# Kernel optimization log

Measured on AMD Instinct MI355X. Metric: run time of the kernel, lower is better.

The kernel has to match this reference:

```python
import jax, jax.numpy as jnp
import numpy as np

B, S, DIM, N, D = 1, 3072, 2048, 16, 128
EPS = 1e-06


def rms_norm(x, w, eps=EPS):
    # x: [B, S, C]; normalize over last dim (matches npu_rms_norm)
    var = jnp.mean(jnp.square(x), axis=-1, keepdims=True)
    return x * jax.lax.rsqrt(var + eps) * w


def rope_interleave(x, cos, sin):
    # x: [B, S, N, D]; cos/sin: [B, S, 1, D] with pairwise-repeated values.
    # interleave mode: (x0, x1) -> (x0*c - x1*s, x1*c + x0*s) for adjacent pairs.
    xe = x[..., 0::2]
    xo = x[..., 1::2]
    rot = jnp.stack([-xo, xe], axis=-1).reshape(x.shape)
    return (x * cos + rot * sin).astype(jnp.float32)  # rope_apply casts to float


def setup_inputs() -> dict:
    key = jax.random.key(0)
    ks = jax.random.split(key, 16)
    sd = 1.0 / np.sqrt(DIM)
    inp = {
        'x': jax.random.normal(ks[0], (B, S, DIM), jnp.float32),
        'Wq': jax.random.normal(ks[1], (DIM, DIM), jnp.float32) * sd,
        'bq': jax.random.normal(ks[2], (DIM,), jnp.float32) * 0.01,
        'Wk': jax.random.normal(ks[3], (DIM, DIM), jnp.float32) * sd,
        'bk': jax.random.normal(ks[4], (DIM,), jnp.float32) * 0.01,
        'Wv': jax.random.normal(ks[5], (DIM, DIM), jnp.float32) * sd,
        'bv': jax.random.normal(ks[6], (DIM,), jnp.float32) * 0.01,
        'Wo': jax.random.normal(ks[7], (DIM, DIM), jnp.float32) * sd,
        'bo': jax.random.normal(ks[8], (DIM,), jnp.float32) * 0.01,
        'norm_q_w': jnp.ones((DIM,), jnp.float32),
        'norm_k_w': jnp.ones((DIM,), jnp.float32),
    }
    # per-sample 3D rope folded into precomputed interleaved cos/sin tables
    pos = jnp.arange(S, dtype=jnp.float32)
    inv = 1.0 / (10000.0 ** (jnp.arange(D // 2, dtype=jnp.float32) / (D // 2)))
    ang = pos[:, None] * inv[None, :]                    # [S, D/2]
    cos = jnp.repeat(jnp.cos(ang), 2, axis=-1)           # [S, D] pairwise repeated
    sin = jnp.repeat(jnp.sin(ang), 2, axis=-1)
    inp['rope_cos'] = jnp.broadcast_to(cos[None, :, None, :], (B, S, 1, D))
    inp['rope_sin'] = jnp.broadcast_to(sin[None, :, None, :], (B, S, 1, D))
    inp['seq_lens'] = jax.random.randint(ks[9], (B,), S // 2, S + 1).astype(jnp.int32)
    inp['grid_sizes'] = jnp.broadcast_to(jnp.array([[12, 16, 16]], jnp.int32), (B, 3))
    return inp


def reference(x, Wq, bq, Wk, bk, Wv, bv, Wo, bo, norm_q_w, norm_k_w,
              rope_cos, rope_sin, seq_lens, grid_sizes):
    b, s, _ = x.shape
    # fused QKV projection + RMSNorm on q/k
    q = rms_norm(x @ Wq.T + bq, norm_q_w).reshape(b, s, N, D)
    k = rms_norm(x @ Wk.T + bk, norm_k_w).reshape(b, s, N, D)
    v = (x @ Wv.T + bv).reshape(b, s, N, D)
    # per-sample interleaved RoPE (outputs float32, as in rope_apply)
    q = rope_interleave(q, rope_cos, rope_sin)
    k = rope_interleave(k, rope_cos, rope_sin)
    # full attention with key-length masking (window_size = (-1, -1))
    scale = 1.0 / np.sqrt(D)
    scores = jnp.einsum('bqnd,bknd->bnqk', q, k) * scale    # [B, N, S, S]
    kmask = jnp.arange(s)[None, :] < seq_lens[:, None]       # [B, S]
    scores = jnp.where(kmask[:, None, None, :], scores, jnp.float32(-1e30))
    probs = jax.nn.softmax(scores, axis=-1)
    out = jnp.einsum('bnqk,bknd->bqnd', probs, v.astype(jnp.float32))
    out = out.reshape(b, s, N * D)
    return out @ Wo.T + bo
```

## Files before the change

kernel.cpp:

```cpp
#include <hip/hip_runtime.h>
#include <hip/hip_bf16.h>

typedef __attribute__((ext_vector_type(8))) short short8;
typedef __attribute__((ext_vector_type(4))) float f32x4;

#define SQ 3072
#define DM 2048
#define NHEAD 16
#define HDIM 128

__device__ __forceinline__ unsigned short f2bf(float f) {
  union { float f; unsigned int u; } un; un.f = f;
  unsigned int r = un.u + 0x7fffu + ((un.u >> 16) & 1u);
  return (unsigned short)(r >> 16);
}

__device__ __forceinline__ unsigned short f2bf_hw(float f) {
  __hip_bfloat16 h = __float2bfloat16(f);
  return *reinterpret_cast<unsigned short*>(&h);
}

__device__ __forceinline__ void gload_lds16(const void* g, void* l) {
  __builtin_amdgcn_global_load_lds(
      (const __attribute__((address_space(1))) void*)g,
      (__attribute__((address_space(3))) void*)l, 16, 0, 0);
}

__global__ __launch_bounds__(256) void cvt_all(
    const float* __restrict__ x, const float* __restrict__ wq, const float* __restrict__ wk,
    const float* __restrict__ wv, const float* __restrict__ wo,
    unsigned short* __restrict__ xb, unsigned short* __restrict__ wqkvb,
    unsigned short* __restrict__ wob)
{
  int b = blockIdx.x;
  const float* src; unsigned short* dst; int idx;
  if (b < 3072) { src = x; dst = xb; idx = b; }
  else {
    int r = b - 3072; int w = r >> 11; idx = r & 2047;
    src = (w == 0) ? wq : (w == 1) ? wk : (w == 2) ? wv : wo;
    dst = (w < 3) ? wqkvb + (size_t)w * DM * DM : wob;
  }
  int i = (idx * 256 + threadIdx.x) * 8;
  float4 a = *(const float4*)(src + i);
  float4 c = *(const float4*)(src + i + 4);
  short8 r;
  r[0] = (short)f2bf(a.x); r[1] = (short)f2bf(a.y);
  r[2] = (short)f2bf(a.z); r[3] = (short)f2bf(a.w);
  r[4] = (short)f2bf(c.x); r[5] = (short)f2bf(c.y);
  r[6] = (short)f2bf(c.z); r[7] = (short)f2bf(c.w);
  *(short8*)(dst + i) = r;
}

__global__ __launch_bounds__(512, 2) void gemm_nt_bias(
    const unsigned short* __restrict__ A, const unsigned short* __restrict__ B,
    const float* __restrict__ b0, const float* __restrict__ b1, const float* __restrict__ b2,
    float* __restrict__ C, int M, int N, int K, int nbm)
{
  __shared__ __align__(16) unsigned short lds[3 * 12288];
  const int tid = threadIdx.x;
  const int w = tid >> 6, l = tid & 63;
  const int wm = w >> 2, wn = w & 3;
  const int lr = l & 15, lg = l >> 4;

  const int nwg = gridDim.x;
  const int swz = (blockIdx.x & 7) * (nwg >> 3) + (blockIdx.x >> 3);
  const int m0 = (swz % nbm) * 128, n0 = (swz / nbm) * 256;

  const int srow = tid >> 2;
  const int scol = ((tid & 3) ^ ((tid >> 3) & 3)) * 8;
  const unsigned short* aS  = A + (size_t)(m0 + srow) * K + scol;
  const unsigned short* bS0 = B + (size_t)(n0 + srow) * K + scol;
  const unsigned short* bS1 = B + (size_t)(n0 + 128 + srow) * K + scol;
  const int ldst = w * 512;

  auto stage = [&](int t, int b) {
    unsigned short* base = &lds[b * 12288];
    const size_t tc = (size_t)t * 32;
    gload_lds16(aS + tc, base + ldst);
    gload_lds16(bS0 + tc, base + 4096 + ldst);
    gload_lds16(bS1 + tc, base + 8192 + ldst);
  };

  const int sx = ((lr >> 1) & 3);
  const int aoff = (wm * 64 + lr) * 32 + ((lg ^ sx) * 8);
  const int boff = 4096 + (wn * 64 + lr) * 32 + ((lg ^ sx) * 8);

  f32x4 acc[4][4] = {};
  const int nt = K >> 5;

  stage(0, 0); stage(1, 1);
  asm volatile("s_waitcnt vmcnt(3)" ::: "memory");
  __builtin_amdgcn_s_barrier();

  for (int t = 0; t < nt; ++t) {
    const unsigned short* buf = &lds[(t % 3) * 12288];
    if (t + 2 < nt) stage(t + 2, (t + 2) % 3);
    short8 af[4], bfr[4];
    #pragma unroll
    for (int m = 0; m < 4; ++m) af[m] = *(const short8*)&buf[aoff + m * 512];
    #pragma unroll
    for (int n = 0; n < 4; ++n) bfr[n] = *(const short8*)&buf[boff + n * 512];
    __builtin_amdgcn_s_setprio(1);
    #pragma unroll
    for (int m = 0; m < 4; ++m) {
      #pragma unroll
      for (int n = 0; n < 4; ++n)
        acc[m][n] = __builtin_amdgcn_mfma_f32_16x16x32_bf16(af[m], bfr[n], acc[m][n], 0, 0, 0);
    }
    __builtin_amdgcn_s_setprio(0);
    if (t + 2 < nt) {
      asm volatile("s_waitcnt vmcnt(3)" ::: "memory");
      __builtin_amdgcn_s_barrier();
    } else if (t + 2 == nt) {
      asm volatile("s_waitcnt vmcnt(0)" ::: "memory");
      __builtin_amdgcn_s_barrier();
    }
  }

  const float* bp = (n0 < DM) ? b0 : ((n0 < 2 * DM) ? b1 : b2);
  #pragma unroll
  for (int n = 0; n < 4; ++n) {
    int col = n0 + wn * 64 + n * 16 + lr;
    float bv = bp[col & (DM - 1)];
    #pragma unroll
    for (int m = 0; m < 4; ++m) {
      int row = m0 + wm * 64 + m * 16 + lg * 4;
      #pragma unroll
      for (int j = 0; j < 4; ++j)
        C[(size_t)(row + j) * N + col] = acc[m][n][j] + bv;
    }
  }
}

__global__ __launch_bounds__(256) void normrope(
    const float* __restrict__ qkv, const float* __restrict__ nqw, const float* __restrict__ nkw,
    const float* __restrict__ cosb, const float* __restrict__ sinb,
    unsigned short* __restrict__ Qb, unsigned short* __restrict__ Kb)
{
  const int s = blockIdx.x, z = blockIdx.y;
  const float* row = qkv + ((size_t)s * 3 + z) * DM;
  const float* gw = z ? nkw : nqw;
  unsigned short* ob = z ? Kb : Qb;
  const int t = threadIdx.x;
  float v[8];
  {
    float4 a = *(const float4*)(row + t * 8);
    float4 b = *(const float4*)(row + t * 8 + 4);
    v[0] = a.x; v[1] = a.y; v[2] = a.z; v[3] = a.w;
    v[4] = b.x; v[5] = b.y; v[6] = b.z; v[7] = b.w;
  }
  float ss = 0.f;
  #pragma unroll
  for (int i = 0; i < 8; ++i) ss += v[i] * v[i];
  #pragma unroll
  for (int off = 1; off < 64; off <<= 1) ss += __shfl_xor(ss, off);
  __shared__ float red[4];
  const int wave = t >> 6, lane = t & 63;
  if (lane == 0) red[wave] = ss;
  __syncthreads();
  float tot = red[0] + red[1] + red[2] + red[3];
  float rsc = rsqrtf(tot * (1.0f / 2048.0f) + 1e-6f);
  const float qs = z ? 1.0f : 0.12751879522087045f;
  const int col = t * 8, d = col & 127, h = col >> 7;
  const float* cb = cosb + (size_t)s * HDIM + d;
  const float* sb = sinb + (size_t)s * HDIM + d;
  float y[8];
  #pragma unroll
  for (int i = 0; i < 8; ++i) y[i] = v[i] * rsc * gw[col + i];
  short8 r;
  #pragma unroll
  for (int p = 0; p < 4; ++p) {
    float e = y[2 * p], o = y[2 * p + 1];
    float c0 = cb[2 * p], s0 = sb[2 * p];
    float c1 = cb[2 * p + 1], s1 = sb[2 * p + 1];
    r[2 * p]     = (short)f2bf((e * c0 - o * s0) * qs);
    r[2 * p + 1] = (short)f2bf((o * c1 + e * s1) * qs);
  }
  *(short8*)(ob + ((size_t)h * SQ + s) * HDIM + d) = r;
}

__global__ __launch_bounds__(256) void vtrans(const float* __restrict__ V, int ldv,
                                              unsigned short* __restrict__ Vt)
{
  __shared__ float tile[64][65];
  const int db = blockIdx.x * 64, sb = blockIdx.y * 64, h = blockIdx.z;
  const int t = threadIdx.x;
  const int rr = t >> 2, c0 = (t & 3) * 16;
  const float* src = V + (size_t)(sb + rr) * ldv + h * HDIM + db + c0;
  #pragma unroll
  for (int i = 0; i < 4; ++i) {
    float4 a = *(const float4*)(src + i * 4);
    tile[rr][c0 + i * 4 + 0] = a.x; tile[rr][c0 + i * 4 + 1] = a.y;
    tile[rr][c0 + i * 4 + 2] = a.z; tile[rr][c0 + i * 4 + 3] = a.w;
  }
  __syncthreads();
  const int dr = t >> 2, s0 = (t & 3) * 16;
  short8 r0, r1;
  #pragma unroll
  for (int i = 0; i < 8; ++i) r0[i] = (short)f2bf(tile[s0 + i][dr]);
  #pragma unroll
  for (int i = 0; i < 8; ++i) r1[i] = (short)f2bf(tile[s0 + 8 + i][dr]);
  unsigned short* dst = Vt + ((size_t)h * HDIM + db + dr) * SQ + sb + s0;
  *(short8*)(dst) = r0;
  *(short8*)(dst + 8) = r1;
}

#define PST 76
__global__ __launch_bounds__(256) void attn(
    const unsigned short* __restrict__ Qb, const unsigned short* __restrict__ Kb,
    const unsigned short* __restrict__ Vt, const int* __restrict__ seq_lens,
    unsigned short* __restrict__ aout)
{
  __shared__ __align__(16) unsigned short Ks[64 * 136];
  __shared__ __align__(16) unsigned short Vs[128 * 72];
  __shared__ __align__(16) unsigned short Ps[4][16 * PST];
  const int tid = threadIdx.x, wave = tid >> 6, lane = tid & 63;
  const int h = blockIdx.y, q0 = blockIdx.x * 64;
  const int lr = lane & 15, lg = lane >> 4;
  const int seq_len = seq_lens[0];

  short8 qf[4];
  {
    const unsigned short* qrow = Qb + ((size_t)h * SQ + q0 + wave * 16 + lr) * HDIM;
    #pragma unroll
    for (int kk = 0; kk < 4; ++kk)
      qf[kk] = *(const short8*)(qrow + kk * 32 + lg * 8);
  }
  f32x4 o[8] = {};
  float lsum[4] = {0.f, 0.f, 0.f, 0.f};

  const unsigned short* kSrc = Kb + ((size_t)h * SQ + (tid >> 4)) * HDIM + (tid & 15) * 8;
  const unsigned short* vSrc = Vt + ((size_t)h * HDIM + (tid >> 3)) * SQ + (tid & 7) * 8;
  unsigned short* kDst = &Ks[(tid >> 4) * 136 + (tid & 15) * 8];
  unsigned short* vDst = &Vs[(tid >> 3) * 72 + (tid & 7) * 8];

  short8 kreg[4], vreg[4];
  #pragma unroll
  for (int c = 0; c < 4; ++c) {
    kreg[c] = *(const short8*)(kSrc + (size_t)c * 16 * HDIM);
    vreg[c] = *(const short8*)(vSrc + (size_t)c * 32 * SQ);
  }

  for (int kt = 0; kt < seq_len; kt += 64) {
    #pragma unroll
    for (int c = 0; c < 4; ++c) {
      *(short8*)(kDst + c * 16 * 136) = kreg[c];
      *(short8*)(vDst + c * 32 * 72) = vreg[c];
    }
    if (kt + 64 < seq_len) {
      #pragma unroll
      for (int c = 0; c < 4; ++c) {
        kreg[c] = *(const short8*)(kSrc + ((size_t)(kt + 64) + c * 16) * HDIM);
        vreg[c] = *(const short8*)(vSrc + (size_t)(kt + 64) + (size_t)c * 32 * SQ);
      }
    }
    __syncthreads();

    f32x4 sf[4] = {};
    __builtin_amdgcn_s_setprio(1);
    #pragma unroll
    for (int kk = 0; kk < 4; ++kk) {
      #pragma unroll
      for (int n = 0; n < 4; ++n) {
        short8 kf = *(const short8*)&Ks[(n * 16 + lr) * 136 + kk * 32 + lg * 8];
        sf[n] = __builtin_amdgcn_mfma_f32_16x16x32_bf16(qf[kk], kf, sf[n], 0, 0, 0);
      }
    }
    __builtin_amdgcn_s_setprio(0);
    if (kt + 64 > seq_len) {
      #pragma unroll
      for (int n = 0; n < 4; ++n) {
        if (kt + n * 16 + lr >= seq_len) {
          #pragma unroll
          for (int j = 0; j < 4; ++j) sf[n][j] = -3.0e38f;
        }
      }
    }
    unsigned short* Pw = &Ps[wave][0];
    #pragma unroll
    for (int n = 0; n < 4; ++n) {
      #pragma unroll
      for (int j = 0; j < 4; ++j) {
        float p = __builtin_amdgcn_exp2f(sf[n][j]);
        lsum[j] += p;
        Pw[(lg * 4 + j) * PST + n * 16 + lr] = f2bf_hw(p);
      }
    }
    #pragma unroll
    for (int kk = 0; kk < 2; ++kk) {
      short8 pa = *(const short8*)&Pw[lr * PST + kk * 32 + lg * 8];
      __builtin_amdgcn_s_setprio(1);
      #pragma unroll
      for (int dn = 0; dn < 8; ++dn) {
        short8 vb = *(const short8*)&Vs[(dn * 16 + lr) * 72 + kk * 32 + lg * 8];
        o[dn] = __builtin_amdgcn_mfma_f32_16x16x32_bf16(pa, vb, o[dn], 0, 0, 0);
      }
      __builtin_amdgcn_s_setprio(0);
    }
    __syncthreads();
  }
  #pragma unroll
  for (int off = 1; off < 16; off <<= 1) {
    #pragma unroll
    for (int j = 0; j < 4; ++j) lsum[j] += __shfl_xor(lsum[j], off);
  }
  float rcp[4];
  #pragma unroll
  for (int j = 0; j < 4; ++j) rcp[j] = 1.0f / lsum[j];
  #pragma unroll
  for (int dn = 0; dn < 8; ++dn) {
    int col = h * HDIM + dn * 16 + lr;
    #pragma unroll
    for (int j = 0; j < 4; ++j) {
      int row = q0 + wave * 16 + lg * 4 + j;
      aout[(size_t)row * DM + col] = f2bf_hw(o[dn][j] * rcp[j]);
    }
  }
}

extern "C" void kernel_launch(void* const* d_in, const int* in_sizes, int n_in,
                              void* d_out, int out_size, void* d_ws, size_t ws_size,
                              hipStream_t stream) {
  const float* x   = (const float*)d_in[0];
  const float* Wq  = (const float*)d_in[1];
  const float* bq  = (const float*)d_in[2];
  const float* Wk  = (const float*)d_in[3];
  const float* bk  = (const float*)d_in[4];
  const float* Wv  = (const float*)d_in[5];
  const float* bv  = (const float*)d_in[6];
  const float* Wo  = (const float*)d_in[7];
  const float* bo  = (const float*)d_in[8];
  const float* nqw = (const float*)d_in[9];
  const float* nkw = (const float*)d_in[10];
  const float* rc  = (const float*)d_in[11];
  const float* rs  = (const float*)d_in[12];
  const int* seql  = (const int*)d_in[13];
  float* out = (float*)d_out;

  unsigned short* xb   = (unsigned short*)d_ws;
  unsigned short* Wqkv = xb   + (size_t)SQ * DM;
  unsigned short* Wob  = Wqkv + (size_t)3 * DM * DM;
  float* qkv           = (float*)(Wob + (size_t)DM * DM);
  unsigned short* Qb   = (unsigned short*)(qkv + (size_t)3 * SQ * DM);
  unsigned short* Kb   = Qb + (size_t)SQ * DM;
  unsigned short* Vt   = Kb + (size_t)SQ * DM;
  unsigned short* aob  = Vt + (size_t)SQ * DM;

  cvt_all<<<3072 + 4 * 2048, 256, 0, stream>>>(x, Wq, Wk, Wv, Wo, xb, Wqkv, Wob);

  gemm_nt_bias<<<(SQ / 128) * (3 * DM / 256), 512, 0, stream>>>(
      xb, Wqkv, bq, bk, bv, qkv, SQ, 3 * DM, DM, SQ / 128);

  normrope<<<dim3(SQ, 2), 256, 0, stream>>>(qkv, nqw, nkw, rc, rs, Qb, Kb);
  vtrans<<<dim3(2, SQ / 64, NHEAD), 256, 0, stream>>>(qkv + 2 * DM, 3 * DM, Vt);

  attn<<<dim3(SQ / 64, NHEAD), 256, 0, stream>>>(Qb, Kb, Vt, seql, aob);

  gemm_nt_bias<<<(SQ / 128) * (DM / 256), 512, 0, stream>>>(
      aob, Wob, bo, bo, bo, out, SQ, DM, DM, SQ / 128);
}
```

Measured before the change: 425.0 us.

## Process two 16-row query sub-tiles per wave to double K/V tile reuse

```diff
diff --git a/kernel.cpp b/kernel.cpp
--- a/kernel.cpp
+++ b/kernel.cpp
@@ -206,28 +206,30 @@
 }
 
 #define PST 76
-__global__ __launch_bounds__(256) void attn(
+__global__ __launch_bounds__(256, 2) void attn(
     const unsigned short* __restrict__ Qb, const unsigned short* __restrict__ Kb,
     const unsigned short* __restrict__ Vt, const int* __restrict__ seq_lens,
     unsigned short* __restrict__ aout)
 {
   __shared__ __align__(16) unsigned short Ks[64 * 136];
   __shared__ __align__(16) unsigned short Vs[128 * 72];
-  __shared__ __align__(16) unsigned short Ps[4][16 * PST];
+  __shared__ __align__(16) unsigned short Ps[4][2][16 * PST];
   const int tid = threadIdx.x, wave = tid >> 6, lane = tid & 63;
-  const int h = blockIdx.y, q0 = blockIdx.x * 64;
+  const int h = blockIdx.y, q0 = blockIdx.x * 128;
   const int lr = lane & 15, lg = lane >> 4;
   const int seq_len = seq_lens[0];
 
-  short8 qf[4];
-  {
-    const unsigned short* qrow = Qb + ((size_t)h * SQ + q0 + wave * 16 + lr) * HDIM;
+  short8 qf[2][4];
+  #pragma unroll
+  for (int s = 0; s < 2; ++s) {
+    const unsigned short* qrow =
+        Qb + ((size_t)h * SQ + q0 + wave * 32 + s * 16 + lr) * HDIM;
     #pragma unroll
     for (int kk = 0; kk < 4; ++kk)
-      qf[kk] = *(const short8*)(qrow + kk * 32 + lg * 8);
-  }
-  f32x4 o[8] = {};
-  float lsum[4] = {0.f, 0.f, 0.f, 0.f};
+      qf[s][kk] = *(const short8*)(qrow + kk * 32 + lg * 8);
+  }
+  f32x4 o[2][8] = {};
+  float lsum[2][4] = {};
 
   const unsigned short* kSrc = Kb + ((size_t)h * SQ + (tid >> 4)) * HDIM + (tid & 15) * 8;
   const unsigned short* vSrc = Vt + ((size_t)h * HDIM + (tid >> 3)) * SQ + (tid & 7) * 8;
@@ -256,14 +258,15 @@
     }
     __syncthreads();
 
-    f32x4 sf[4] = {};
+    f32x4 sf[2][4] = {};
     __builtin_amdgcn_s_setprio(1);
     #pragma unroll
     for (int kk = 0; kk < 4; ++kk) {
       #pragma unroll
       for (int n = 0; n < 4; ++n) {
         short8 kf = *(const short8*)&Ks[(n * 16 + lr) * 136 + kk * 32 + lg * 8];
-        sf[n] = __builtin_amdgcn_mfma_f32_16x16x32_bf16(qf[kk], kf, sf[n], 0, 0, 0);
+        sf[0][n] = __builtin_amdgcn_mfma_f32_16x16x32_bf16(qf[0][kk], kf, sf[0][n], 0, 0, 0);
+        sf[1][n] = __builtin_amdgcn_mfma_f32_16x16x32_bf16(qf[1][kk], kf, sf[1][n], 0, 0, 0);
       }
     }
     __builtin_amdgcn_s_setprio(0);
@@ -272,28 +275,33 @@
       for (int n = 0; n < 4; ++n) {
         if (kt + n * 16 + lr >= seq_len) {
           #pragma unroll
-          for (int j = 0; j < 4; ++j) sf[n][j] = -3.0e38f;
+          for (int j = 0; j < 4; ++j) { sf[0][n][j] = -3.0e38f; sf[1][n][j] = -3.0e38f; }
         }
       }
     }
-    unsigned short* Pw = &Ps[wave][0];
-    #pragma unroll
-    for (int n = 0; n < 4; ++n) {
-      #pragma unroll
-      for (int j = 0; j < 4; ++j) {
-        float p = __builtin_amdgcn_exp2f(sf[n][j]);
-        lsum[j] += p;
-        Pw[(lg * 4 + j) * PST + n * 16 + lr] = f2bf_hw(p);
+    #pragma unroll
+    for (int s = 0; s < 2; ++s) {
+      unsigned short* Pw = &Ps[wave][s][0];
+      #pragma unroll
+      for (int n = 0; n < 4; ++n) {
+        #pragma unroll
+        for (int j = 0; j < 4; ++j) {
+          float p = __builtin_amdgcn_exp2f(sf[s][n][j]);
+          lsum[s][j] += p;
+          Pw[(lg * 4 + j) * PST + n * 16 + lr] = f2bf_hw(p);
+        }
       }
     }
     #pragma unroll
     for (int kk = 0; kk < 2; ++kk) {
-      short8 pa = *(const short8*)&Pw[lr * PST + kk * 32 + lg * 8];
+      short8 pa0 = *(const short8*)&Ps[wave][0][lr * PST + kk * 32 + lg * 8];
+      short8 pa1 = *(const short8*)&Ps[wave][1][lr * PST + kk * 32 + lg * 8];
       __builtin_amdgcn_s_setprio(1);
       #pragma unroll
       for (int dn = 0; dn < 8; ++dn) {
         short8 vb = *(const short8*)&Vs[(dn * 16 + lr) * 72 + kk * 32 + lg * 8];
-        o[dn] = __builtin_amdgcn_mfma_f32_16x16x32_bf16(pa, vb, o[dn], 0, 0, 0);
+        o[0][dn] = __builtin_amdgcn_mfma_f32_16x16x32_bf16(pa0, vb, o[0][dn], 0, 0, 0);
+        o[1][dn] = __builtin_amdgcn_mfma_f32_16x16x32_bf16(pa1, vb, o[1][dn], 0, 0, 0);
       }
       __builtin_amdgcn_s_setprio(0);
     }
@@ -302,18 +310,24 @@
   #pragma unroll
   for (int off = 1; off < 16; off <<= 1) {
     #pragma unroll
-    for (int j = 0; j < 4; ++j) lsum[j] += __shfl_xor(lsum[j], off);
-  }
-  float rcp[4];
-  #pragma unroll
-  for (int j = 0; j < 4; ++j) rcp[j] = 1.0f / lsum[j];
-  #pragma unroll
-  for (int dn = 0; dn < 8; ++dn) {
-    int col = h * HDIM + dn * 16 + lr;
-    #pragma unroll
-    for (int j = 0; j < 4; ++j) {
-      int row = q0 + wave * 16 + lg * 4 + j;
-      aout[(size_t)row * DM + col] = f2bf_hw(o[dn][j] * rcp[j]);
+    for (int s = 0; s < 2; ++s) {
+      #pragma unroll
+      for (int j = 0; j < 4; ++j) lsum[s][j] += __shfl_xor(lsum[s][j], off);
+    }
+  }
+  #pragma unroll
+  for (int s = 0; s < 2; ++s) {
+    float rcp[4];
+    #pragma unroll
+    for (int j = 0; j < 4; ++j) rcp[j] = 1.0f / lsum[s][j];
+    #pragma unroll
+    for (int dn = 0; dn < 8; ++dn) {
+      int col = h * HDIM + dn * 16 + lr;
+      #pragma unroll
+      for (int j = 0; j < 4; ++j) {
+        int row = q0 + wave * 32 + s * 16 + lg * 4 + j;
+        aout[(size_t)row * DM + col] = f2bf_hw(o[s][dn][j] * rcp[j]);
+      }
     }
   }
 }
@@ -354,7 +368,7 @@
   normrope<<<dim3(SQ, 2), 256, 0, stream>>>(qkv, nqw, nkw, rc, rs, Qb, Kb);
   vtrans<<<dim3(2, SQ / 64, NHEAD), 256, 0, stream>>>(qkv + 2 * DM, 3 * DM, Vt);
 
-  attn<<<dim3(SQ / 64, NHEAD), 256, 0, stream>>>(Qb, Kb, Vt, seql, aob);
+  attn<<<dim3(SQ / 128, NHEAD), 256, 0, stream>>>(Qb, Kb, Vt, seql, aob);
 
   gemm_nt_bias<<<(SQ / 128) * (DM / 256), 512, 0, stream>>>(
       aob, Wob, bo, bo, bo, out, SQ, DM, DM, SQ / 128);
```

New measurement: 396.1 us. -6.8%, faster.
